# Performance work log

Measured on AMD Instinct MI355X. Metric: run time of the kernel, lower is better.

Reference implementation:

```python
import jax, jax.numpy as jnp
import numpy as np

TEMPERATURE = 0.1  # init kwarg
EPS = 1e-8        # torch cosine_similarity eps


def setup_inputs() -> dict:
    key = jax.random.key(0)
    k1, k2, k3 = jax.random.split(key, 3)
    B, D, C = 4096, 1024, 32
    representations = jax.random.normal(k1, (B, D), dtype=jnp.float32)
    soft_labels = jax.random.uniform(k2, (B, C), dtype=jnp.float32)
    labels = jax.random.randint(k3, (B,), 0, 32, dtype=jnp.int64)
    return {
        "representations": representations,
        "soft_labels": soft_labels,
        "labels": labels,
        "pseudo_weight": 10,
    }


def reference(representations, soft_labels, labels, pseudo_weight):
    B = representations.shape[0]
    # row-normalize (cosine similarity)
    norms = jnp.maximum(jnp.linalg.norm(representations, axis=1, keepdims=True), EPS)
    rn = representations / norms
    Z = (rn @ rn.T) / TEMPERATURE                      # [B, B] scaled cosine sims
    E = jnp.exp(Z)
    off_diag = 1.0 - jnp.eye(B, dtype=Z.dtype)         # exclude j == i
    denom = jnp.sum(E * off_diag, axis=1, keepdims=True)   # [B, 1]
    loss_arr = -(Z - jnp.log(denom))                   # -log(exp(Z_ij)/denom_i)
    # positive-pair weights: same label, j != i (detached in original)
    pos = (labels[:, None] == labels[None, :]).astype(Z.dtype) * off_diag
    soft_sim = jax.lax.stop_gradient(soft_labels @ soft_labels.T)  # torch.inner, detached
    w = pos + pseudo_weight * soft_sim
    return jnp.sum(loss_arr * w) / B
```

## Files before the change

### kernel.cpp

```cpp
#include <hip/hip_runtime.h>
#include <hip/hip_bf16.h>
#include <stdint.h>


typedef float f32x4 __attribute__((ext_vector_type(4)));
typedef long i64;

#define INV_T 10.0f
#define Z_SCALE (INV_T / 256.0f)

#define GLD16(gp, lp)                                                          \
    __builtin_amdgcn_global_load_lds(                                          \
        (const __attribute__((address_space(1))) uint32_t*)(gp),               \
        (__attribute__((address_space(3))) uint32_t*)(lp), 16, 0, 0)

#define OFF_RNF8  0
#define OFF_DENOM 4194304
#define OFF_POSS  (OFF_DENOM + 16384)
#define OFF_G     (OFF_POSS + 16384)
#define OFF_OACC  (OFF_G + 131072)
#define OFF_DONE  (OFF_OACC + 16)
#define ZERO_SPAN 167936
#define OFF_CSP   (OFF_DENOM + ZERO_SPAN)
#define OFF_CCP   (OFF_CSP + 4096)
#define OFF_W     (OFF_CCP + 4096)

#define N_GEMM 1056
#define N_G    512
#define N_ALL  (N_GEMM + N_G + 16)

__global__ __launch_bounds__(256) void scl_stage1(const float* __restrict__ rep,
                                                  const float* __restrict__ sl,
                                                  const int* __restrict__ labels,
                                                  uint32_t* __restrict__ rnf8,
                                                  float* __restrict__ cs_part,
                                                  int* __restrict__ cc_part,
                                                  char* __restrict__ zbase) {
    int b = blockIdx.x;
    int t = threadIdx.x;
    if (b < 4096) {
        int row = b;
        const float4* src = reinterpret_cast<const float4*>(rep + (size_t)row * 1024);
        float4 v = src[t];
        float s = v.x * v.x + v.y * v.y + v.z * v.z + v.w * v.w;
#pragma unroll
        for (int m = 1; m < 64; m <<= 1) s += __shfl_xor(s, m, 64);
        __shared__ float red[4];
        if ((t & 63) == 0) red[t >> 6] = s;
        __syncthreads();
        s = red[0] + red[1] + red[2] + red[3];
        float nf = 16.0f / fmaxf(sqrtf(s), 1e-8f);
        int p = 0;
        p = __builtin_amdgcn_cvt_pk_fp8_f32(v.x * nf, v.y * nf, p, false);
        p = __builtin_amdgcn_cvt_pk_fp8_f32(v.z * nf, v.w * nf, p, true);
        rnf8[row * 256 + t] = (uint32_t)p;
    } else if (b < 4128) {
        __shared__ float part[8][32];
        __shared__ int bins[32];
        int bb = b - 4096;
        if (t < 32) bins[t] = 0;
        __syncthreads();
        if (t < 128) atomicAdd(&bins[labels[bb * 128 + t]], 1);
        int c = t & 31, rg = t >> 5;
        float s = 0.f;
#pragma unroll 4
        for (int k = 0; k < 16; ++k) {
            int i = bb * 128 + rg * 16 + k;
            s += sl[i * 32 + c];
        }
        part[rg][c] = s;
        __syncthreads();
        if (t < 32) {
            float tot = 0.f;
#pragma unroll
            for (int g = 0; g < 8; ++g) tot += part[g][t];
            cs_part[bb * 32 + t] = tot;
            cc_part[bb * 32 + t] = bins[t];
        }
    } else {
        int zb = b - 4128;
        *(uint4*)(zbase + (size_t)zb * 4096 + t * 16) = (uint4){0, 0, 0, 0};
    }
}

__global__ __launch_bounds__(256) void scl_main(const uint8_t* __restrict__ rnf8,
                                                const float* __restrict__ sl,
                                                const int* __restrict__ labels,
                                                const float* __restrict__ cs_part,
                                                const int* __restrict__ cc_part,
                                                const int* __restrict__ pwp,
                                                float* __restrict__ denom,
                                                float* __restrict__ posS,
                                                float* __restrict__ G,
                                                float* __restrict__ W) {
    int tid = threadIdx.x;
    int bIdx = blockIdx.x;

    if (bIdx >= N_GEMM) {
        if (bIdx < N_GEMM + N_G) {
            int idx = bIdx - N_GEMM;
            int dblk = idx & 15, ks = idx >> 4;
            int dq = tid >> 5, c = tid & 31;
            int d0 = dblk * 64 + dq * 8;
            float acc[8];
#pragma unroll
            for (int j = 0; j < 8; ++j) acc[j] = 0.f;
            int i0 = ks * 128;
#pragma unroll 4
            for (int k = 0; k < 128; ++k) {
                int i = i0 + k;
                uint2 rv = *(const uint2*)&rnf8[(size_t)i * 1024 + d0];
                float sv = sl[i * 32 + c];
                acc[0] += __builtin_amdgcn_cvt_f32_fp8((int)rv.x, 0) * sv;
                acc[1] += __builtin_amdgcn_cvt_f32_fp8((int)rv.x, 1) * sv;
                acc[2] += __builtin_amdgcn_cvt_f32_fp8((int)rv.x, 2) * sv;
                acc[3] += __builtin_amdgcn_cvt_f32_fp8((int)rv.x, 3) * sv;
                acc[4] += __builtin_amdgcn_cvt_f32_fp8((int)rv.y, 0) * sv;
                acc[5] += __builtin_amdgcn_cvt_f32_fp8((int)rv.y, 1) * sv;
                acc[6] += __builtin_amdgcn_cvt_f32_fp8((int)rv.y, 2) * sv;
                acc[7] += __builtin_amdgcn_cvt_f32_fp8((int)rv.y, 3) * sv;
            }
#pragma unroll
            for (int j = 0; j < 8; ++j)
                atomicAdd(&G[(d0 + j) * 32 + c], acc[j] * 0.0625f);
        } else {
            __shared__ __align__(16) float css[32];
            __shared__ int ccs[32];
            if (tid < 32) {
                float s = 0.f; int n = 0;
#pragma unroll
                for (int b = 0; b < 32; ++b) { s += cs_part[b * 32 + tid]; n += cc_part[b * 32 + tid]; }
                css[tid] = s; ccs[tid] = n;
            }
            __syncthreads();
            int bits = *pwp;
            float pw = (bits >= -(1 << 22) && bits <= (1 << 22)) ? (float)bits
                                                                 : __int_as_float(bits);
            int i = (bIdx - (N_GEMM + N_G)) * 256 + tid;
            const f32x4* sl4 = (const f32x4*)sl;
            const f32x4* cs4 = (const f32x4*)css;
            float dW = 0.f;
#pragma unroll
            for (int q = 0; q < 8; ++q) {
                f32x4 s = sl4[i * 8 + q];
                f32x4 c = cs4[q];
                dW += s[0] * c[0] + s[1] * c[1] + s[2] * c[2] + s[3] * c[3];
            }
            W[i] = (float)(ccs[labels[i]] - 1) + pw * dW;
        }
        return;
    }

    __shared__ __align__(16) uint8_t As[2][128 * 64];
    __shared__ __align__(16) uint8_t Bs[2][64 * 64];
    __shared__ int lblA[128];
    __shared__ int lblB[64];

    int L = (bIdx & 7) * 132 + (bIdx >> 3);
    int bi = 0, rem = L;
    while (rem >= 64 - 2 * bi) { rem -= 64 - 2 * bi; ++bi; }
    int bj = 2 * bi + rem;
    int rowA0 = bi * 128, colB0 = bj * 64;
    bool doCol = (bj >= 2 * bi + 2);

    if (tid < 128) lblA[tid] = labels[rowA0 + tid];
    else if (tid < 192) lblB[tid - 128] = labels[colB0 + (tid - 128)];

    int lane = tid & 63, warp = tid >> 6;
    int wr = warp >> 1, wc = warp & 1;
    int m_ = lane & 15, g = lane >> 4;

    int r4 = lane >> 2;
    int csw = (lane & 3) ^ ((lane >> 3) & 3);
    const uint8_t* gA0 = rnf8 + (size_t)(rowA0 + warp * 32 + r4) * 1024 + csw * 16;
    const uint8_t* gB0 = rnf8 + (size_t)(colB0 + warp * 16 + r4) * 1024 + csw * 16;

    f32x4 acc[4][2];
#pragma unroll
    for (int a = 0; a < 4; ++a)
#pragma unroll
        for (int b = 0; b < 2; ++b) acc[a][b] = (f32x4){0.f, 0.f, 0.f, 0.f};

    int fsw = (g ^ ((m_ >> 1) & 3)) * 16;

    GLD16(gA0,         &As[0][(warp * 32) * 64]);
    GLD16(gA0 + 16384, &As[0][(warp * 32 + 16) * 64]);
    GLD16(gB0,         &Bs[0][(warp * 16) * 64]);

    for (int kt = 0; kt < 16; ++kt) {
        int cur = kt & 1;
        __syncthreads();
        f32x4 aq[4], bq[2];
#pragma unroll
        for (int ti = 0; ti < 4; ++ti) {
            int rowLoc = wr * 64 + ti * 16 + m_;
            aq[ti] = *(const f32x4*)&As[cur][rowLoc * 64 + fsw];
        }
#pragma unroll
        for (int tj = 0; tj < 2; ++tj) {
            int colLoc = wc * 32 + tj * 16 + m_;
            bq[tj] = *(const f32x4*)&Bs[cur][colLoc * 64 + fsw];
        }
        if (kt < 15) {
            int nxt = cur ^ 1;
            GLD16(gA0 + (kt + 1) * 64,         &As[nxt][(warp * 32) * 64]);
            GLD16(gA0 + (kt + 1) * 64 + 16384, &As[nxt][(warp * 32 + 16) * 64]);
            GLD16(gB0 + (kt + 1) * 64,         &Bs[nxt][(warp * 16) * 64]);
        }
#pragma unroll
        for (int s = 0; s < 2; ++s)
#pragma unroll
            for (int ti = 0; ti < 4; ++ti)
#pragma unroll
                for (int tj = 0; tj < 2; ++tj) {
                    i64 a = ((const i64*)&aq[ti])[s];
                    i64 b = ((const i64*)&bq[tj])[s];
                    acc[ti][tj] = __builtin_amdgcn_mfma_f32_16x16x32_fp8_fp8(
                        a, b, acc[ti][tj], 0, 0, 0);
                }
    }

    int cl = m_;
    float colE[2] = {0.f, 0.f}, colP[2] = {0.f, 0.f};
#pragma unroll
    for (int ti = 0; ti < 4; ++ti) {
        int rowLoc = wr * 64 + ti * 16 + g * 4;
        float rE[4] = {0.f, 0.f, 0.f, 0.f}, rP[4] = {0.f, 0.f, 0.f, 0.f};
        int lr[4];
#pragma unroll
        for (int r = 0; r < 4; ++r) lr[r] = lblA[rowLoc + r];
#pragma unroll
        for (int tj = 0; tj < 2; ++tj) {
            int colLoc = wc * 32 + tj * 16 + cl;
            int gCol = colB0 + colLoc;
            int lc = lblB[colLoc];
            f32x4 a = acc[ti][tj];
#pragma unroll
            for (int r = 0; r < 4; ++r) {
                int gRow = rowA0 + rowLoc + r;
                float z = Z_SCALE * a[r];
                float e = __expf(z);
                bool offd = (gRow != gCol);
                if (!offd) e = 0.f;
                rE[r] += e;
                colE[tj] += e;
                if (offd && (lr[r] == lc)) { rP[r] += z; colP[tj] += z; }
            }
        }
#pragma unroll
        for (int r = 0; r < 4; ++r) {
            float v = rE[r], p = rP[r];
#pragma unroll
            for (int msk = 1; msk < 16; msk <<= 1) {
                v += __shfl_xor(v, msk, 64);
                p += __shfl_xor(p, msk, 64);
            }
            if (cl == 0) {
                int gRow = rowA0 + rowLoc + r;
                atomicAdd(&denom[gRow], v);
                atomicAdd(&posS[gRow], p);
            }
        }
    }
    if (doCol) {
#pragma unroll
        for (int tj = 0; tj < 2; ++tj) {
            float v = colE[tj], p = colP[tj];
            v += __shfl_xor(v, 16, 64); p += __shfl_xor(p, 16, 64);
            v += __shfl_xor(v, 32, 64); p += __shfl_xor(p, 32, 64);
            if (g == 0) {
                int gCol = colB0 + wc * 32 + tj * 16 + cl;
                atomicAdd(&denom[gCol], v);
                atomicAdd(&posS[gCol], p);
            }
        }
    }
}

__global__ __launch_bounds__(256) void scl_finalize(const float* __restrict__ denom,
                                                    const float* __restrict__ posS,
                                                    const float* __restrict__ W,
                                                    const float* __restrict__ G,
                                                    const int* __restrict__ pwp,
                                                    double* __restrict__ oacc,
                                                    int* __restrict__ done,
                                                    float* __restrict__ out) {
    int t = threadIdx.x;
    __shared__ double wsum[4];
    double contrib = 0.0;

    if (blockIdx.x < 8) {
        int i0 = blockIdx.x * 512 + t;
        float t0 = __logf(denom[i0]) * W[i0] - posS[i0];
        float t1 = __logf(denom[i0 + 256]) * W[i0 + 256] - posS[i0 + 256];
        double td = (double)t0 + (double)t1;
#pragma unroll
        for (int m = 1; m < 64; m <<= 1) td += __shfl_xor(td, m, 64);
        if ((t & 63) == 0) wsum[t >> 6] = td;
        __syncthreads();
        contrib = wsum[0] + wsum[1] + wsum[2] + wsum[3];
    } else {
        int bits = *pwp;
        float pw = (bits >= -(1 << 22) && bits <= (1 << 22)) ? (float)bits
                                                             : __int_as_float(bits);
        const f32x4* G4 = (const f32x4*)G;
        float gs = 0.f;
#pragma unroll
        for (int q = 0; q < 32; ++q) {
            f32x4 v = G4[q * 256 + t];
            gs += v[0] * v[0] + v[1] * v[1] + v[2] * v[2] + v[3] * v[3];
        }
        double gd = (double)gs;
#pragma unroll
        for (int m = 1; m < 64; m <<= 1) gd += __shfl_xor(gd, m, 64);
        if ((t & 63) == 0) wsum[t >> 6] = gd;
        __syncthreads();
        contrib = -(double)(pw * INV_T) * (wsum[0] + wsum[1] + wsum[2] + wsum[3]);
    }

    if (t == 0) {
        atomicAdd(oacc, contrib);
        __threadfence();
        int old = atomicAdd(done, 1);
        if (old == 8) {
            double tot = atomicAdd(oacc, 0.0);
            out[0] = (float)(tot * (1.0 / 4096.0));
        }
    }
}

extern "C" void kernel_launch(void* const* d_in, const int* in_sizes, int n_in,
                              void* d_out, int out_size, void* d_ws, size_t ws_size,
                              hipStream_t stream) {
    const float* rep = (const float*)d_in[0];
    const float* sl = (const float*)d_in[1];
    const int* labels = (const int*)d_in[2];
    const int* pwp = (const int*)d_in[3];

    char* ws = (char*)d_ws;
    uint8_t* rnf8 = (uint8_t*)(ws + OFF_RNF8);
    float* denom = (float*)(ws + OFF_DENOM);
    float* posS = (float*)(ws + OFF_POSS);
    float* G = (float*)(ws + OFF_G);
    double* oacc = (double*)(ws + OFF_OACC);
    int* done = (int*)(ws + OFF_DONE);
    float* cs_part = (float*)(ws + OFF_CSP);
    int* cc_part = (int*)(ws + OFF_CCP);
    float* W = (float*)(ws + OFF_W);

    scl_stage1<<<4169, 256, 0, stream>>>(rep, sl, labels, (uint32_t*)rnf8,
                                         cs_part, cc_part, ws + OFF_DENOM);
    scl_main<<<N_ALL, 256, 0, stream>>>(rnf8, sl, labels, cs_part, cc_part, pwp,
                                        denom, posS, G, W);
    scl_finalize<<<9, 256, 0, stream>>>(denom, posS, W, G, pwp, oacc, done,
                                        (float*)d_out);
}
```

Baseline: 126.5 us.

## Switch symmetric Gram tiles to 128x128 with 512-thread blocks

Measured after the change: 134.8 us. +6.5%, slower.

```diff
diff --git a/kernel.cpp b/kernel.cpp
--- a/kernel.cpp
+++ b/kernel.cpp
@@ -25,9 +25,10 @@
 #define OFF_CCP   (OFF_CSP + 4096)
 #define OFF_W     (OFF_CCP + 4096)
 
-#define N_GEMM 1056
+#define N_GEMM 528
 #define N_G    512
-#define N_ALL  (N_GEMM + N_G + 16)
+#define N_W    8
+#define N_ALL  (N_GEMM + N_G + N_W)
 
 __global__ __launch_bounds__(256) void scl_stage1(const float* __restrict__ rep,
                                                   const float* __restrict__ sl,
@@ -83,16 +84,16 @@
     }
 }
 
-__global__ __launch_bounds__(256) void scl_main(const uint8_t* __restrict__ rnf8,
-                                                const float* __restrict__ sl,
-                                                const int* __restrict__ labels,
-                                                const float* __restrict__ cs_part,
-                                                const int* __restrict__ cc_part,
-                                                const int* __restrict__ pwp,
-                                                float* __restrict__ denom,
-                                                float* __restrict__ posS,
-                                                float* __restrict__ G,
-                                                float* __restrict__ W) {
+__global__ __launch_bounds__(512, 4) void scl_main(const uint8_t* __restrict__ rnf8,
+                                                   const float* __restrict__ sl,
+                                                   const int* __restrict__ labels,
+                                                   const float* __restrict__ cs_part,
+                                                   const int* __restrict__ cc_part,
+                                                   const int* __restrict__ pwp,
+                                                   float* __restrict__ denom,
+                                                   float* __restrict__ posS,
+                                                   float* __restrict__ G,
+                                                   float* __restrict__ W) {
     int tid = threadIdx.x;
     int bIdx = blockIdx.x;
 
@@ -101,27 +102,23 @@
             int idx = bIdx - N_GEMM;
             int dblk = idx & 15, ks = idx >> 4;
             int dq = tid >> 5, c = tid & 31;
-            int d0 = dblk * 64 + dq * 8;
-            float acc[8];
-#pragma unroll
-            for (int j = 0; j < 8; ++j) acc[j] = 0.f;
+            int d0 = dblk * 64 + dq * 4;
+            float acc[4];
+#pragma unroll
+            for (int j = 0; j < 4; ++j) acc[j] = 0.f;
             int i0 = ks * 128;
 #pragma unroll 4
             for (int k = 0; k < 128; ++k) {
                 int i = i0 + k;
-                uint2 rv = *(const uint2*)&rnf8[(size_t)i * 1024 + d0];
+                uint32_t rv = *(const uint32_t*)&rnf8[(size_t)i * 1024 + d0];
                 float sv = sl[i * 32 + c];
-                acc[0] += __builtin_amdgcn_cvt_f32_fp8((int)rv.x, 0) * sv;
-                acc[1] += __builtin_amdgcn_cvt_f32_fp8((int)rv.x, 1) * sv;
-                acc[2] += __builtin_amdgcn_cvt_f32_fp8((int)rv.x, 2) * sv;
-                acc[3] += __builtin_amdgcn_cvt_f32_fp8((int)rv.x, 3) * sv;
-                acc[4] += __builtin_amdgcn_cvt_f32_fp8((int)rv.y, 0) * sv;
-                acc[5] += __builtin_amdgcn_cvt_f32_fp8((int)rv.y, 1) * sv;
-                acc[6] += __builtin_amdgcn_cvt_f32_fp8((int)rv.y, 2) * sv;
-                acc[7] += __builtin_amdgcn_cvt_f32_fp8((int)rv.y, 3) * sv;
-            }
-#pragma unroll
-            for (int j = 0; j < 8; ++j)
+                acc[0] += __builtin_amdgcn_cvt_f32_fp8((int)rv, 0) * sv;
+                acc[1] += __builtin_amdgcn_cvt_f32_fp8((int)rv, 1) * sv;
+                acc[2] += __builtin_amdgcn_cvt_f32_fp8((int)rv, 2) * sv;
+                acc[3] += __builtin_amdgcn_cvt_f32_fp8((int)rv, 3) * sv;
+            }
+#pragma unroll
+            for (int j = 0; j < 4; ++j)
                 atomicAdd(&G[(d0 + j) * 32 + c], acc[j] * 0.0625f);
         } else {
             __shared__ __align__(16) float css[32];
@@ -136,7 +133,7 @@
             int bits = *pwp;
             float pw = (bits >= -(1 << 22) && bits <= (1 << 22)) ? (float)bits
                                                                  : __int_as_float(bits);
-            int i = (bIdx - (N_GEMM + N_G)) * 256 + tid;
+            int i = (bIdx - (N_GEMM + N_G)) * 512 + tid;
             const f32x4* sl4 = (const f32x4*)sl;
             const f32x4* cs4 = (const f32x4*)css;
             float dW = 0.f;
@@ -152,27 +149,25 @@
     }
 
     __shared__ __align__(16) uint8_t As[2][128 * 64];
-    __shared__ __align__(16) uint8_t Bs[2][64 * 64];
-    __shared__ int lblA[128];
-    __shared__ int lblB[64];
-
-    int L = (bIdx & 7) * 132 + (bIdx >> 3);
+    __shared__ __align__(16) uint8_t Bs[2][128 * 64];
+    __shared__ int lblA[128], lblB[128];
+
+    int L = (bIdx & 7) * 66 + (bIdx >> 3);
     int bi = 0, rem = L;
-    while (rem >= 64 - 2 * bi) { rem -= 64 - 2 * bi; ++bi; }
-    int bj = 2 * bi + rem;
-    int rowA0 = bi * 128, colB0 = bj * 64;
-    bool doCol = (bj >= 2 * bi + 2);
+    while (rem >= 32 - bi) { rem -= 32 - bi; ++bi; }
+    int bj = bi + rem;
+    int rowA0 = bi * 128, colB0 = bj * 128;
 
     if (tid < 128) lblA[tid] = labels[rowA0 + tid];
-    else if (tid < 192) lblB[tid - 128] = labels[colB0 + (tid - 128)];
+    else if (tid < 256) lblB[tid - 128] = labels[colB0 + (tid - 128)];
 
     int lane = tid & 63, warp = tid >> 6;
-    int wr = warp >> 1, wc = warp & 1;
+    int wr = warp >> 2, wc = warp & 3;
     int m_ = lane & 15, g = lane >> 4;
 
     int r4 = lane >> 2;
     int csw = (lane & 3) ^ ((lane >> 3) & 3);
-    const uint8_t* gA0 = rnf8 + (size_t)(rowA0 + warp * 32 + r4) * 1024 + csw * 16;
+    const uint8_t* gA0 = rnf8 + (size_t)(rowA0 + warp * 16 + r4) * 1024 + csw * 16;
     const uint8_t* gB0 = rnf8 + (size_t)(colB0 + warp * 16 + r4) * 1024 + csw * 16;
 
     f32x4 acc[4][2];
@@ -183,9 +178,8 @@
 
     int fsw = (g ^ ((m_ >> 1) & 3)) * 16;
 
-    GLD16(gA0,         &As[0][(warp * 32) * 64]);
-    GLD16(gA0 + 16384, &As[0][(warp * 32 + 16) * 64]);
-    GLD16(gB0,         &Bs[0][(warp * 16) * 64]);
+    GLD16(gA0, &As[0][(warp * 16) * 64]);
+    GLD16(gB0, &Bs[0][(warp * 16) * 64]);
 
     for (int kt = 0; kt < 16; ++kt) {
         int cur = kt & 1;
@@ -203,9 +197,8 @@
         }
         if (kt < 15) {
             int nxt = cur ^ 1;
-            GLD16(gA0 + (kt + 1) * 64,         &As[nxt][(warp * 32) * 64]);
-            GLD16(gA0 + (kt + 1) * 64 + 16384, &As[nxt][(warp * 32 + 16) * 64]);
-            GLD16(gB0 + (kt + 1) * 64,         &Bs[nxt][(warp * 16) * 64]);
+            GLD16(gA0 + (kt + 1) * 64, &As[nxt][(warp * 16) * 64]);
+            GLD16(gB0 + (kt + 1) * 64, &Bs[nxt][(warp * 16) * 64]);
         }
 #pragma unroll
         for (int s = 0; s < 2; ++s)
@@ -220,6 +213,7 @@
                 }
     }
 
+    bool isDiag = (bi == bj);
     int cl = m_;
     float colE[2] = {0.f, 0.f}, colP[2] = {0.f, 0.f};
 #pragma unroll
@@ -262,7 +256,7 @@
             }
         }
     }
-    if (doCol) {
+    if (!isDiag) {
 #pragma unroll
         for (int tj = 0; tj < 2; ++tj) {
             float v = colE[tj], p = colP[tj];
@@ -350,7 +344,7 @@
 
     scl_stage1<<<4169, 256, 0, stream>>>(rep, sl, labels, (uint32_t*)rnf8,
                                          cs_part, cc_part, ws + OFF_DENOM);
-    scl_main<<<N_ALL, 256, 0, stream>>>(rnf8, sl, labels, cs_part, cc_part, pwp,
+    scl_main<<<N_ALL, 512, 0, stream>>>(rnf8, sl, labels, cs_part, cc_part, pwp,
                                         denom, posS, G, W);
     scl_finalize<<<9, 256, 0, stream>>>(denom, posS, W, G, pwp, oacc, done,
                                         (float*)d_out);
```
